# Optimization experiments

Hardware: AMD Instinct MI355X
Metric: run time of the kernel (lower is better)

## Reference

```python
import jax, jax.numpy as jnp
import numpy as np

N_AGENTS = 32
STATE_DIM = 512
EMBED = 64
BATCH = 32768


def setup_inputs() -> dict:
    key = jax.random.key(0)
    ks = jax.random.split(key, 16)
    g = lambda k, shape, fan_in: jax.random.normal(k, shape, jnp.float32) / np.sqrt(fan_in)
    return {
        "agent_qs": jax.random.normal(ks[0], (BATCH, N_AGENTS), jnp.float32),
        "states": jax.random.normal(ks[1], (BATCH, STATE_DIM), jnp.float32),
        # hyper_w1: Linear(state,E) -> ReLU -> Linear(E, n_agents*E)
        "w1_l1_w": g(ks[2], (EMBED, STATE_DIM), STATE_DIM),
        "w1_l1_b": jnp.zeros((EMBED,), jnp.float32),
        "w1_l2_w": g(ks[3], (N_AGENTS * EMBED, EMBED), EMBED),
        "w1_l2_b": jnp.zeros((N_AGENTS * EMBED,), jnp.float32),
        # hyper_w2: Linear(state,E) -> ReLU -> Linear(E, E)
        "w2_l1_w": g(ks[4], (EMBED, STATE_DIM), STATE_DIM),
        "w2_l1_b": jnp.zeros((EMBED,), jnp.float32),
        "w2_l2_w": g(ks[5], (EMBED, EMBED), EMBED),
        "w2_l2_b": jnp.zeros((EMBED,), jnp.float32),
        # hyper_b1: Linear(state, E)
        "b1_w": g(ks[6], (EMBED, STATE_DIM), STATE_DIM),
        "b1_b": jnp.zeros((EMBED,), jnp.float32),
        # hyper_b2: Linear(state,E) -> ReLU -> Linear(E, 1)
        "b2_l1_w": g(ks[7], (EMBED, STATE_DIM), STATE_DIM),
        "b2_l1_b": jnp.zeros((EMBED,), jnp.float32),
        "b2_l2_w": g(ks[8], (1, EMBED), EMBED),
        "b2_l2_b": jnp.zeros((1,), jnp.float32),
    }


def _linear(x, w, b):
    return x @ w.T + b


def reference(agent_qs, states,
              w1_l1_w, w1_l1_b, w1_l2_w, w1_l2_b,
              w2_l1_w, w2_l1_b, w2_l2_w, w2_l2_b,
              b1_w, b1_b, b2_l1_w, b2_l1_b, b2_l2_w, b2_l2_b):
    B = agent_qs.shape[0]
    # hypernetworks producing per-sample weights
    w1 = jnp.abs(_linear(jax.nn.relu(_linear(states, w1_l1_w, w1_l1_b)), w1_l2_w, w1_l2_b))
    w1 = w1.reshape(B, N_AGENTS, EMBED)                      # [B, A, E]
    b1 = _linear(states, b1_w, b1_b)                         # [B, E]
    hidden = jax.nn.elu(jnp.einsum('ba,bae->be', agent_qs, w1) + b1)  # [B, E]
    w2 = jnp.abs(_linear(jax.nn.relu(_linear(states, w2_l1_w, w2_l1_b)), w2_l2_w, w2_l2_b))  # [B, E]
    b2 = _linear(jax.nn.relu(_linear(states, b2_l1_w, b2_l1_b)), b2_l2_w, b2_l2_b)           # [B, 1]
    q_total = jnp.einsum('be,be->b', hidden, w2) + b2[:, 0]  # [B]
    return q_total
```

## Files before the change

kernel.cpp:

```cpp
#include <hip/hip_runtime.h>

typedef unsigned short u16;
typedef unsigned int u32;
typedef short bf16x8 __attribute__((ext_vector_type(8)));
typedef float f32x4 __attribute__((ext_vector_type(4)));
typedef u16 u16x4 __attribute__((ext_vector_type(4)));

#define NAG 32
#define STATE 512
#define EMBED 64
#define TB 64

#define OFF_W1L1 0
#define OFF_W2L1 32768
#define OFF_B1W  65536
#define OFF_B2L1 98304
#define OFF_W1L2 131072
#define OFF_W2L2 262144
#define WS_TOTAL 266240

#define WBUF_OFF 0
#define SB_OFF   16384
#define SB_STR   72
#define QST_OFF  20992
#define QST_STR  68
#define W1BS_OFF 23168
#define Y_OFF    25216
#define Y_STR    200
#define PBUF_OFF 0
#define PBUF_STR 72
#define PBUF_WV  (64 * 72)
#define QACC_OFF  38016
#define QACC2_OFF 38144
#define B2WV_OFF  38272
#define SMEM_U16  38400

__device__ __forceinline__ float bf2f(u16 u) {
    u32 i = ((u32)u) << 16; float f;
    __builtin_memcpy(&f, &i, 4); return f;
}
__device__ __forceinline__ u16 f2bf(float f) {
    u32 i; __builtin_memcpy(&i, &f, 4);
    return (u16)((i + 0x8000u) >> 16);
}
__device__ __forceinline__ bf16x8 ld8(const u16* p) {
    return *reinterpret_cast<const bf16x8*>(p);
}
__device__ __forceinline__ bf16x8 cvt8(f32x4 a, f32x4 b) {
    bf16x8 r;
#pragma unroll
    for (int i = 0; i < 4; ++i) r[i]     = (short)f2bf(a[i]);
#pragma unroll
    for (int i = 0; i < 4; ++i) r[i + 4] = (short)f2bf(b[i]);
    return r;
}
__device__ __forceinline__ void dma16(const void* g, void* l) {
    __builtin_amdgcn_global_load_lds(
        (const __attribute__((address_space(1))) u32*)g,
        (__attribute__((address_space(3))) u32*)l, 16, 0, 0);
}

__global__ __launch_bounds__(256) void cvt_weights(
    const float* __restrict__ w1l1w, const float* __restrict__ w2l1w,
    const float* __restrict__ b1w,   const float* __restrict__ b2l1w,
    const float* __restrict__ w1l2w, const float* __restrict__ w2l2w,
    u16* __restrict__ ws)
{
    int idx = blockIdx.x * 256 + threadIdx.x;
    const float* src; int off;
    if      (idx < OFF_W2L1)  { src = w1l1w; off = OFF_W1L1; }
    else if (idx < OFF_B1W)   { src = w2l1w; off = OFF_W2L1; }
    else if (idx < OFF_B2L1)  { src = b1w;   off = OFF_B1W;  }
    else if (idx < OFF_W1L2)  { src = b2l1w; off = OFF_B2L1; }
    else if (idx < OFF_W2L2)  { src = w1l2w; off = OFF_W1L2; }
    else if (idx < WS_TOTAL)  { src = w2l2w; off = OFF_W2L2; }
    else return;
    ws[idx] = f2bf(src[idx - off]);
}

__global__ __launch_bounds__(256, 2) void qmix_kernel(
    const float* __restrict__ qs,    const float* __restrict__ st,
    const u16*  __restrict__ wsb,
    const float* __restrict__ w1l1b, const float* __restrict__ w1l2b,
    const float* __restrict__ w2l1b, const float* __restrict__ w2l2b,
    const float* __restrict__ b1b,   const float* __restrict__ b2l1b,
    const float* __restrict__ b2l2w, const float* __restrict__ b2l2b,
    float* __restrict__ out)
{
    __shared__ u16 smem[SMEM_U16];
    float* qaccF  = (float*)(smem + QACC_OFF);
    float* qacc2F = (float*)(smem + QACC2_OFF);
    float* b2wvF  = (float*)(smem + B2WV_OFF);

    const int t    = threadIdx.x;
    const int wave = t >> 6, lane = t & 63;
    const int m = lane & 15, quad = lane >> 4;
    const int rsub = lane >> 3, cch = lane & 7;
    const int sc = cch ^ rsub;
    const int sbase = blockIdx.x * TB;

    if (t < 64) b2wvF[t] = b2l2w[t];
    {
        const float* qp = qs + (size_t)sbase * NAG + t * 8;
        f32x4 q0 = *reinterpret_cast<const f32x4*>(qp);
        f32x4 q1 = *reinterpret_cast<const f32x4*>(qp + 4);
        const int s = t >> 2, a0 = (t & 3) * 8;
#pragma unroll
        for (int j = 0; j < 4; ++j) smem[QST_OFF + (a0 + j) * QST_STR + s]     = f2bf(q0[j]);
#pragma unroll
        for (int j = 0; j < 4; ++j) smem[QST_OFF + (a0 + 4 + j) * QST_STR + s] = f2bf(q1[j]);
        f32x4 w0 = *reinterpret_cast<const f32x4*>(w1l2b + t * 8);
        f32x4 w1 = *reinterpret_cast<const f32x4*>(w1l2b + t * 8 + 4);
        *reinterpret_cast<bf16x8*>(&smem[W1BS_OFF + t * 8]) = cvt8(w0, w1);
    }

    const int ss1 = t >> 3, c8 = t & 7;
    const float* stb = st + (size_t)sbase * STATE;

    f32x4 acc[4][4] = {};
    for (int ks = 0; ks < 8; ++ks) {
        __syncthreads();
#pragma unroll
        for (int j = 0; j < 8; ++j)
            dma16(wsb + (size_t)(wave * 64 + j * 8 + rsub) * STATE + ks * 64 + sc * 8,
                  &smem[WBUF_OFF + (wave * 64 + j * 8) * 64]);
        {
            const float* g1 = stb + (size_t)ss1 * STATE + ks * 64 + c8 * 8;
            const float* g2 = g1 + (size_t)32 * STATE;
            f32x4 a0 = *reinterpret_cast<const f32x4*>(g1);
            f32x4 a1 = *reinterpret_cast<const f32x4*>(g1 + 4);
            f32x4 a2 = *reinterpret_cast<const f32x4*>(g2);
            f32x4 a3 = *reinterpret_cast<const f32x4*>(g2 + 4);
            *reinterpret_cast<bf16x8*>(&smem[SB_OFF + ss1 * SB_STR + c8 * 8])        = cvt8(a0, a1);
            *reinterpret_cast<bf16x8*>(&smem[SB_OFF + (ss1 + 32) * SB_STR + c8 * 8]) = cvt8(a2, a3);
        }
        __builtin_amdgcn_s_waitcnt(0);
        __syncthreads();
        bf16x8 wfr[4][2];
#pragma unroll
        for (int ot = 0; ot < 4; ++ot) {
            const int brow = wave * 64 + ot * 16 + m;
            wfr[ot][0] = ld8(&smem[WBUF_OFF + brow * 64 + ((quad ^ (brow & 7))) * 8]);
            wfr[ot][1] = ld8(&smem[WBUF_OFF + brow * 64 + (((quad + 4) ^ (brow & 7))) * 8]);
        }
#pragma unroll
        for (int st2 = 0; st2 < 4; ++st2) {
            const int row = st2 * 16 + m;
            bf16x8 af0 = ld8(&smem[SB_OFF + row * SB_STR + quad * 8]);
            bf16x8 af1 = ld8(&smem[SB_OFF + row * SB_STR + (quad + 4) * 8]);
#pragma unroll
            for (int ot = 0; ot < 4; ++ot)
                acc[st2][ot] = __builtin_amdgcn_mfma_f32_16x16x32_bf16(af0, wfr[ot][0], acc[st2][ot], 0, 0, 0);
#pragma unroll
            for (int ot = 0; ot < 4; ++ot)
                acc[st2][ot] = __builtin_amdgcn_mfma_f32_16x16x32_bf16(af1, wfr[ot][1], acc[st2][ot], 0, 0, 0);
        }
    }

    if (wave < 3) {
        const float* barr = (wave == 0) ? w1l1b : (wave == 1) ? w2l1b : b1b;
        const bool isrelu = (wave != 2);
        float wb[4];
#pragma unroll
        for (int ot = 0; ot < 4; ++ot) wb[ot] = barr[ot * 16 + m];
#pragma unroll
        for (int st2 = 0; st2 < 4; ++st2)
#pragma unroll
            for (int ot = 0; ot < 4; ++ot)
#pragma unroll
                for (int r = 0; r < 4; ++r) {
                    float v = acc[st2][ot][r] + wb[ot];
                    if (isrelu) v = fmaxf(v, 0.f);
                    smem[Y_OFF + (st2 * 16 + quad * 4 + r) * Y_STR + wave * 64 + ot * 16 + m] = f2bf(v);
                }
    } else {
        float wb[4], bw[4];
#pragma unroll
        for (int ot = 0; ot < 4; ++ot) wb[ot] = b2l1b[ot * 16 + m];
#pragma unroll
        for (int ot = 0; ot < 4; ++ot) bw[ot] = b2wvF[ot * 16 + m];
#pragma unroll
        for (int st2 = 0; st2 < 4; ++st2)
#pragma unroll
            for (int r = 0; r < 4; ++r) {
                float pd = 0.f;
#pragma unroll
                for (int ot = 0; ot < 4; ++ot)
                    pd += fmaxf(acc[st2][ot][r] + wb[ot], 0.f) * bw[ot];
#pragma unroll
                for (int off = 1; off < 16; off <<= 1) pd += __shfl_xor(pd, off, 64);
                if (m == 0) qacc2F[st2 * 16 + quad * 4 + r] = pd;
            }
    }
    __syncthreads();

    bf16x8 h1f[4][2];
#pragma unroll
    for (int st2 = 0; st2 < 4; ++st2) {
        h1f[st2][0] = ld8(&smem[Y_OFF + (st2 * 16 + m) * Y_STR + quad * 8]);
        h1f[st2][1] = ld8(&smem[Y_OFF + (st2 * 16 + m) * Y_STR + 32 + quad * 8]);
    }

    f32x4 hacc[4][4] = {};
    for (int j = 0; j < 8; ++j) {
        __syncthreads();
        const int a = wave * 8 + j;
#pragma unroll
        for (int jj = 0; jj < 8; ++jj)
            dma16(wsb + OFF_W1L2 + (size_t)(a * 64 + jj * 8 + rsub) * EMBED + sc * 8,
                  &smem[WBUF_OFF + (wave * 64 + jj * 8) * 64]);
        __builtin_amdgcn_s_waitcnt(0);
        __syncthreads();
        bf16x8 wf[4][2];
#pragma unroll
        for (int tp = 0; tp < 4; ++tp) {
            const int brow = wave * 64 + tp * 16 + m;
            wf[tp][0] = ld8(&smem[WBUF_OFF + brow * 64 + ((quad ^ (brow & 7))) * 8]);
            wf[tp][1] = ld8(&smem[WBUF_OFF + brow * 64 + (((quad + 4) ^ (brow & 7))) * 8]);
        }
        float bias[4];
#pragma unroll
        for (int tp = 0; tp < 4; ++tp) bias[tp] = bf2f(smem[W1BS_OFF + a * EMBED + tp * 16 + m]);
#pragma unroll
        for (int st2 = 0; st2 < 4; ++st2) {
            u16x4 qv = *reinterpret_cast<const u16x4*>(
                &smem[QST_OFF + a * QST_STR + st2 * 16 + quad * 4]);
#pragma unroll
            for (int tp = 0; tp < 4; ++tp) {
                f32x4 p = {};
                p = __builtin_amdgcn_mfma_f32_16x16x32_bf16(h1f[st2][0], wf[tp][0], p, 0, 0, 0);
                p = __builtin_amdgcn_mfma_f32_16x16x32_bf16(h1f[st2][1], wf[tp][1], p, 0, 0, 0);
#pragma unroll
                for (int r = 0; r < 4; ++r)
                    hacc[st2][tp][r] += bf2f((u16)qv[r]) * fabsf(p[r] + bias[tp]);
            }
        }
    }
    __syncthreads();

#pragma unroll
    for (int st2 = 0; st2 < 4; ++st2)
#pragma unroll
        for (int tp = 0; tp < 4; ++tp)
#pragma unroll
            for (int r = 0; r < 4; ++r)
                smem[PBUF_OFF + wave * PBUF_WV
                     + (st2 * 16 + quad * 4 + r) * PBUF_STR + tp * 16 + m]
                    = f2bf(hacc[st2][tp][r]);
    __syncthreads();

    {
        const int s  = wave * 16 + (lane & 15);
        const int eb = (lane >> 4) * 16;
        float v[16];
#pragma unroll
        for (int jj = 0; jj < 16; ++jj) v[jj] = 0.f;
#pragma unroll
        for (int pw = 0; pw < 4; ++pw) {
#pragma unroll
            for (int c = 0; c < 4; ++c) {
                u16x4 x = *reinterpret_cast<const u16x4*>(
                    &smem[PBUF_OFF + pw * PBUF_WV + s * PBUF_STR + eb + c * 4]);
#pragma unroll
                for (int jj = 0; jj < 4; ++jj) v[c * 4 + jj] += bf2f((u16)x[jj]);
            }
        }
        bf16x8 bv0 = ld8(&smem[Y_OFF + s * Y_STR + 128 + eb]);
        bf16x8 bv1 = ld8(&smem[Y_OFF + s * Y_STR + 128 + eb + 8]);
        bf16x8 o0, o1;
#pragma unroll
        for (int jj = 0; jj < 8; ++jj) {
            float h0 = v[jj] + bf2f((u16)bv0[jj]);
            h0 = (h0 > 0.f) ? h0 : (__expf(h0) - 1.f);
            o0[jj] = (short)f2bf(h0);
            float h1 = v[8 + jj] + bf2f((u16)bv1[jj]);
            h1 = (h1 > 0.f) ? h1 : (__expf(h1) - 1.f);
            o1[jj] = (short)f2bf(h1);
        }
        *reinterpret_cast<bf16x8*>(&smem[Y_OFF + s * Y_STR + 128 + eb])     = o0;
        *reinterpret_cast<bf16x8*>(&smem[Y_OFF + s * Y_STR + 128 + eb + 8]) = o1;
    }
    __syncthreads();

    {
        const int s0 = wave * 16;
        bf16x8 h2f0 = ld8(&smem[Y_OFF + (s0 + m) * Y_STR + 64 + quad * 8]);
        bf16x8 h2f1 = ld8(&smem[Y_OFF + (s0 + m) * Y_STR + 96 + quad * 8]);

        f32x4 qp = {};
#pragma unroll
        for (int tp = 0; tp < 4; ++tp) {
            const u16* wc = wsb + OFF_W2L2 + (size_t)(tp * 16 + m) * EMBED + quad * 8;
            bf16x8 c0 = ld8(wc);
            bf16x8 c1 = ld8(wc + 32);
            f32x4 p = {};
            p = __builtin_amdgcn_mfma_f32_16x16x32_bf16(h2f0, c0, p, 0, 0, 0);
            p = __builtin_amdgcn_mfma_f32_16x16x32_bf16(h2f1, c1, p, 0, 0, 0);
            const float bias = w2l2b[tp * 16 + m];
#pragma unroll
            for (int r = 0; r < 4; ++r)
                qp[r] += bf2f(smem[Y_OFF + (s0 + quad * 4 + r) * Y_STR + 128 + tp * 16 + m])
                         * fabsf(p[r] + bias);
        }
#pragma unroll
        for (int off = 1; off < 16; off <<= 1) {
#pragma unroll
            for (int r = 0; r < 4; ++r) qp[r] += __shfl_xor(qp[r], off, 64);
        }
        if (m == 0) {
#pragma unroll
            for (int r = 0; r < 4; ++r) qaccF[s0 + quad * 4 + r] = qp[r];
        }
    }
    __syncthreads();

    if (t < TB) out[sbase + t] = qaccF[t] + qacc2F[t] + b2l2b[0];
}

extern "C" void kernel_launch(void* const* d_in, const int* in_sizes, int n_in,
                              void* d_out, int out_size, void* d_ws, size_t ws_size,
                              hipStream_t stream)
{
    const float* qs    = (const float*)d_in[0];
    const float* st    = (const float*)d_in[1];
    const float* w1l1w = (const float*)d_in[2];
    const float* w1l1b = (const float*)d_in[3];
    const float* w1l2w = (const float*)d_in[4];
    const float* w1l2b = (const float*)d_in[5];
    const float* w2l1w = (const float*)d_in[6];
    const float* w2l1b = (const float*)d_in[7];
    const float* w2l2w = (const float*)d_in[8];
    const float* w2l2b = (const float*)d_in[9];
    const float* b1w   = (const float*)d_in[10];
    const float* b1b   = (const float*)d_in[11];
    const float* b2l1w = (const float*)d_in[12];
    const float* b2l1b = (const float*)d_in[13];
    const float* b2l2w = (const float*)d_in[14];
    const float* b2l2b = (const float*)d_in[15];

    u16* wsb = (u16*)d_ws;

    cvt_weights<<<(WS_TOTAL + 255) / 256, 256, 0, stream>>>(
        w1l1w, w2l1w, b1w, b2l1w, w1l2w, w2l2w, wsb);

    int B = in_sizes[0] / NAG;
    int grid = B / TB;
    qmix_kernel<<<grid, 256, 0, stream>>>(
        qs, st, wsb,
        w1l1b, w1l2b, w2l1b, w2l2b, b1b, b2l1b, b2l2w, b2l2b,
        (float*)d_out);
}
```

Before: 147.5 us.

## Double-buffer weight DMA and state staging across both GEMM loops

Splits each K-step into two half-tiles and double-buffers the weight tiles in LDS, issuing the async copy for the next half-tile before computing on the current one. State rows are prefetched into registers one step ahead and written into a second LDS buffer, and the first W1L2 tile is prefetched during the last state-GEMM step. This removes the wait-all-then-compute pattern per iteration, keeping one barrier per step. The b1 output moves to its own LDS region so the Y buffer shrinks. In exchange it uses more LDS and registers and fully unrolls 16-step loops, which may reduce occupancy or grow code size.

```diff
diff --git a/kernel.cpp b/kernel.cpp
--- a/kernel.cpp
+++ b/kernel.cpp
@@ -20,20 +20,23 @@
 #define WS_TOTAL 266240
 
 #define WBUF_OFF 0
+#define WBUF_SZ  8192
 #define SB_OFF   16384
 #define SB_STR   72
-#define QST_OFF  20992
+#define SB_BUF   4608
+#define B1V_OFF  20992
+#define QST_OFF  25600
 #define QST_STR  68
-#define W1BS_OFF 23168
-#define Y_OFF    25216
-#define Y_STR    200
+#define W1BS_OFF 27776
+#define Y_OFF    29824
+#define Y_STR    136
 #define PBUF_OFF 0
 #define PBUF_STR 72
-#define PBUF_WV  (64 * 72)
-#define QACC_OFF  38016
-#define QACC2_OFF 38144
-#define B2WV_OFF  38272
-#define SMEM_U16  38400
+#define PBUF_WV  4608
+#define QACC_OFF  38528
+#define QACC2_OFF 38656
+#define B2WV_OFF  38784
+#define SMEM_U16  38912
 
 __device__ __forceinline__ float bf2f(u16 u) {
     u32 i = ((u32)u) << 16; float f;
@@ -95,8 +98,8 @@
     const int t    = threadIdx.x;
     const int wave = t >> 6, lane = t & 63;
     const int m = lane & 15, quad = lane >> 4;
-    const int rsub = lane >> 3, cch = lane & 7;
-    const int sc = cch ^ rsub;
+    const int r8 = lane >> 3, c8l = lane & 7;
+    const int scx = c8l ^ r8;
     const int sbase = blockIdx.x * TB;
 
     if (t < 64) b2wvF[t] = b2l2w[t];
@@ -116,67 +119,105 @@
 
     const int ss1 = t >> 3, c8 = t & 7;
     const float* stb = st + (size_t)sbase * STATE;
+    {
+        const float* g1 = stb + (size_t)ss1 * STATE + c8 * 8;
+        const float* g2 = g1 + (size_t)32 * STATE;
+        f32x4 a0 = *reinterpret_cast<const f32x4*>(g1);
+        f32x4 a1 = *reinterpret_cast<const f32x4*>(g1 + 4);
+        f32x4 a2 = *reinterpret_cast<const f32x4*>(g2);
+        f32x4 a3 = *reinterpret_cast<const f32x4*>(g2 + 4);
+        *reinterpret_cast<bf16x8*>(&smem[SB_OFF + ss1 * SB_STR + c8 * 8])        = cvt8(a0, a1);
+        *reinterpret_cast<bf16x8*>(&smem[SB_OFF + (ss1 + 32) * SB_STR + c8 * 8]) = cvt8(a2, a3);
+    }
+#pragma unroll
+    for (int j = 0; j < 4; ++j)
+        dma16(wsb + (size_t)(wave * 64 + j * 8 + r8) * STATE + scx * 8,
+              &smem[WBUF_OFF + (wave * 32 + j * 8) * 64]);
+    __syncthreads();
 
     f32x4 acc[4][4] = {};
-    for (int ks = 0; ks < 8; ++ks) {
-        __syncthreads();
-#pragma unroll
-        for (int j = 0; j < 8; ++j)
-            dma16(wsb + (size_t)(wave * 64 + j * 8 + rsub) * STATE + ks * 64 + sc * 8,
-                  &smem[WBUF_OFF + (wave * 64 + j * 8) * 64]);
-        {
-            const float* g1 = stb + (size_t)ss1 * STATE + ks * 64 + c8 * 8;
+    f32x4 sa[4];
+#pragma unroll
+    for (int s = 0; s < 16; ++s) {
+        const int ks = s >> 1, h = s & 1, cur = s & 1, nxt = cur ^ 1;
+        if (s < 15) {
+            const int ks2 = (s + 1) >> 1, h2 = (s + 1) & 1;
+#pragma unroll
+            for (int j = 0; j < 4; ++j)
+                dma16(wsb + (size_t)(wave * 64 + h2 * 32 + j * 8 + r8) * STATE + ks2 * 64 + scx * 8,
+                      &smem[WBUF_OFF + nxt * WBUF_SZ + (wave * 32 + j * 8) * 64]);
+        } else {
+#pragma unroll
+            for (int j = 0; j < 4; ++j)
+                dma16(wsb + OFF_W1L2 + (size_t)(wave * 8 * 64 + j * 8 + r8) * EMBED + scx * 8,
+                      &smem[WBUF_OFF + nxt * WBUF_SZ + (wave * 32 + j * 8) * 64]);
+        }
+        if (h == 0 && ks < 7) {
+            const float* g1 = stb + (size_t)ss1 * STATE + (ks + 1) * 64 + c8 * 8;
             const float* g2 = g1 + (size_t)32 * STATE;
-            f32x4 a0 = *reinterpret_cast<const f32x4*>(g1);
-            f32x4 a1 = *reinterpret_cast<const f32x4*>(g1 + 4);
-            f32x4 a2 = *reinterpret_cast<const f32x4*>(g2);
-            f32x4 a3 = *reinterpret_cast<const f32x4*>(g2 + 4);
-            *reinterpret_cast<bf16x8*>(&smem[SB_OFF + ss1 * SB_STR + c8 * 8])        = cvt8(a0, a1);
-            *reinterpret_cast<bf16x8*>(&smem[SB_OFF + (ss1 + 32) * SB_STR + c8 * 8]) = cvt8(a2, a3);
-        }
-        __builtin_amdgcn_s_waitcnt(0);
-        __syncthreads();
-        bf16x8 wfr[4][2];
-#pragma unroll
-        for (int ot = 0; ot < 4; ++ot) {
-            const int brow = wave * 64 + ot * 16 + m;
-            wfr[ot][0] = ld8(&smem[WBUF_OFF + brow * 64 + ((quad ^ (brow & 7))) * 8]);
-            wfr[ot][1] = ld8(&smem[WBUF_OFF + brow * 64 + (((quad + 4) ^ (brow & 7))) * 8]);
+            sa[0] = *reinterpret_cast<const f32x4*>(g1);
+            sa[1] = *reinterpret_cast<const f32x4*>(g1 + 4);
+            sa[2] = *reinterpret_cast<const f32x4*>(g2);
+            sa[3] = *reinterpret_cast<const f32x4*>(g2 + 4);
+        }
+        const u16* wb  = &smem[WBUF_OFF + cur * WBUF_SZ];
+        const u16* sbc = &smem[SB_OFF + (ks & 1) * SB_BUF];
+        bf16x8 wf[2][2];
+#pragma unroll
+        for (int o = 0; o < 2; ++o) {
+            const int br = wave * 32 + o * 16 + m;
+            wf[o][0] = ld8(&wb[br * 64 + ((quad ^ (m & 7))) * 8]);
+            wf[o][1] = ld8(&wb[br * 64 + (((quad + 4) ^ (m & 7))) * 8]);
         }
 #pragma unroll
         for (int st2 = 0; st2 < 4; ++st2) {
             const int row = st2 * 16 + m;
-            bf16x8 af0 = ld8(&smem[SB_OFF + row * SB_STR + quad * 8]);
-            bf16x8 af1 = ld8(&smem[SB_OFF + row * SB_STR + (quad + 4) * 8]);
+            bf16x8 af0 = ld8(&sbc[row * SB_STR + quad * 8]);
+            bf16x8 af1 = ld8(&sbc[row * SB_STR + (quad + 4) * 8]);
+#pragma unroll
+            for (int o = 0; o < 2; ++o) {
+                acc[st2][h * 2 + o] = __builtin_amdgcn_mfma_f32_16x16x32_bf16(af0, wf[o][0], acc[st2][h * 2 + o], 0, 0, 0);
+                acc[st2][h * 2 + o] = __builtin_amdgcn_mfma_f32_16x16x32_bf16(af1, wf[o][1], acc[st2][h * 2 + o], 0, 0, 0);
+            }
+        }
+        if (h == 1 && ks < 7) {
+            u16* dst = &smem[SB_OFF + ((ks + 1) & 1) * SB_BUF];
+            *reinterpret_cast<bf16x8*>(&dst[ss1 * SB_STR + c8 * 8])        = cvt8(sa[0], sa[1]);
+            *reinterpret_cast<bf16x8*>(&dst[(ss1 + 32) * SB_STR + c8 * 8]) = cvt8(sa[2], sa[3]);
+        }
+        __syncthreads();
+    }
+
+    if (wave < 2) {
+        const float* barr = (wave == 0) ? w1l1b : w2l1b;
+        float wb4[4];
+#pragma unroll
+        for (int ot = 0; ot < 4; ++ot) wb4[ot] = barr[ot * 16 + m];
+#pragma unroll
+        for (int st2 = 0; st2 < 4; ++st2)
 #pragma unroll
             for (int ot = 0; ot < 4; ++ot)
-                acc[st2][ot] = __builtin_amdgcn_mfma_f32_16x16x32_bf16(af0, wfr[ot][0], acc[st2][ot], 0, 0, 0);
-#pragma unroll
-            for (int ot = 0; ot < 4; ++ot)
-                acc[st2][ot] = __builtin_amdgcn_mfma_f32_16x16x32_bf16(af1, wfr[ot][1], acc[st2][ot], 0, 0, 0);
-        }
-    }
-
-    if (wave < 3) {
-        const float* barr = (wave == 0) ? w1l1b : (wave == 1) ? w2l1b : b1b;
-        const bool isrelu = (wave != 2);
-        float wb[4];
-#pragma unroll
-        for (int ot = 0; ot < 4; ++ot) wb[ot] = barr[ot * 16 + m];
-#pragma unroll
-        for (int st2 = 0; st2 < 4; ++st2)
-#pragma unroll
-            for (int ot = 0; ot < 4; ++ot)
 #pragma unroll
                 for (int r = 0; r < 4; ++r) {
-                    float v = acc[st2][ot][r] + wb[ot];
-                    if (isrelu) v = fmaxf(v, 0.f);
+                    float v = fmaxf(acc[st2][ot][r] + wb4[ot], 0.f);
                     smem[Y_OFF + (st2 * 16 + quad * 4 + r) * Y_STR + wave * 64 + ot * 16 + m] = f2bf(v);
                 }
+    } else if (wave == 2) {
+        float wb4[4];
+#pragma unroll
+        for (int ot = 0; ot < 4; ++ot) wb4[ot] = b1b[ot * 16 + m];
+#pragma unroll
+        for (int st2 = 0; st2 < 4; ++st2)
+#pragma unroll
+            for (int ot = 0; ot < 4; ++ot)
+#pragma unroll
+                for (int r = 0; r < 4; ++r)
+                    smem[B1V_OFF + (st2 * 16 + quad * 4 + r) * SB_STR + ot * 16 + m]
+                        = f2bf(acc[st2][ot][r] + wb4[ot]);
     } else {
-        float wb[4], bw[4];
-#pragma unroll
-        for (int ot = 0; ot < 4; ++ot) wb[ot] = b2l1b[ot * 16 + m];
+        float wb4[4], bw[4];
+#pragma unroll
+        for (int ot = 0; ot < 4; ++ot) wb4[ot] = b2l1b[ot * 16 + m];
 #pragma unroll
         for (int ot = 0; ot < 4; ++ot) bw[ot] = b2wvF[ot * 16 + m];
 #pragma unroll
@@ -186,7 +227,7 @@
                 float pd = 0.f;
 #pragma unroll
                 for (int ot = 0; ot < 4; ++ot)
-                    pd += fmaxf(acc[st2][ot][r] + wb[ot], 0.f) * bw[ot];
+                    pd += fmaxf(acc[st2][ot][r] + wb4[ot], 0.f) * bw[ot];
 #pragma unroll
                 for (int off = 1; off < 16; off <<= 1) pd += __shfl_xor(pd, off, 64);
                 if (m == 0) qacc2F[st2 * 16 + quad * 4 + r] = pd;
@@ -202,41 +243,46 @@
     }
 
     f32x4 hacc[4][4] = {};
-    for (int j = 0; j < 8; ++j) {
-        __syncthreads();
-        const int a = wave * 8 + j;
-#pragma unroll
-        for (int jj = 0; jj < 8; ++jj)
-            dma16(wsb + OFF_W1L2 + (size_t)(a * 64 + jj * 8 + rsub) * EMBED + sc * 8,
-                  &smem[WBUF_OFF + (wave * 64 + jj * 8) * 64]);
-        __builtin_amdgcn_s_waitcnt(0);
-        __syncthreads();
-        bf16x8 wf[4][2];
-#pragma unroll
-        for (int tp = 0; tp < 4; ++tp) {
-            const int brow = wave * 64 + tp * 16 + m;
-            wf[tp][0] = ld8(&smem[WBUF_OFF + brow * 64 + ((quad ^ (brow & 7))) * 8]);
-            wf[tp][1] = ld8(&smem[WBUF_OFF + brow * 64 + (((quad + 4) ^ (brow & 7))) * 8]);
-        }
-        float bias[4];
-#pragma unroll
-        for (int tp = 0; tp < 4; ++tp) bias[tp] = bf2f(smem[W1BS_OFF + a * EMBED + tp * 16 + m]);
+#pragma unroll
+    for (int s = 0; s < 16; ++s) {
+        const int jb = s >> 1, hb = s & 1, cur = s & 1, nxt = cur ^ 1;
+        const int a = wave * 8 + jb;
+        if (s < 15) {
+            const int jb2 = (s + 1) >> 1, hb2 = (s + 1) & 1;
+            const int a2 = wave * 8 + jb2;
+#pragma unroll
+            for (int j = 0; j < 4; ++j)
+                dma16(wsb + OFF_W1L2 + (size_t)(a2 * 64 + hb2 * 32 + j * 8 + r8) * EMBED + scx * 8,
+                      &smem[WBUF_OFF + nxt * WBUF_SZ + (wave * 32 + j * 8) * 64]);
+        }
+        const u16* wb = &smem[WBUF_OFF + cur * WBUF_SZ];
+        bf16x8 wf[2][2];
+#pragma unroll
+        for (int o = 0; o < 2; ++o) {
+            const int br = wave * 32 + o * 16 + m;
+            wf[o][0] = ld8(&wb[br * 64 + ((quad ^ (m & 7))) * 8]);
+            wf[o][1] = ld8(&wb[br * 64 + (((quad + 4) ^ (m & 7))) * 8]);
+        }
+        float bias2[2];
+#pragma unroll
+        for (int o = 0; o < 2; ++o)
+            bias2[o] = bf2f(smem[W1BS_OFF + a * EMBED + (hb * 2 + o) * 16 + m]);
 #pragma unroll
         for (int st2 = 0; st2 < 4; ++st2) {
             u16x4 qv = *reinterpret_cast<const u16x4*>(
                 &smem[QST_OFF + a * QST_STR + st2 * 16 + quad * 4]);
 #pragma unroll
-            for (int tp = 0; tp < 4; ++tp) {
+            for (int o = 0; o < 2; ++o) {
                 f32x4 p = {};
-                p = __builtin_amdgcn_mfma_f32_16x16x32_bf16(h1f[st2][0], wf[tp][0], p, 0, 0, 0);
-                p = __builtin_amdgcn_mfma_f32_16x16x32_bf16(h1f[st2][1], wf[tp][1], p, 0, 0, 0);
+                p = __builtin_amdgcn_mfma_f32_16x16x32_bf16(h1f[st2][0], wf[o][0], p, 0, 0, 0);
+                p = __builtin_amdgcn_mfma_f32_16x16x32_bf16(h1f[st2][1], wf[o][1], p, 0, 0, 0);
 #pragma unroll
                 for (int r = 0; r < 4; ++r)
-                    hacc[st2][tp][r] += bf2f((u16)qv[r]) * fabsf(p[r] + bias[tp]);
+                    hacc[st2][hb * 2 + o][r] += bf2f((u16)qv[r]) * fabsf(p[r] + bias2[o]);
             }
         }
-    }
-    __syncthreads();
+        __syncthreads();
+    }
 
 #pragma unroll
     for (int st2 = 0; st2 < 4; ++st2)
@@ -265,8 +311,8 @@
                 for (int jj = 0; jj < 4; ++jj) v[c * 4 + jj] += bf2f((u16)x[jj]);
             }
         }
-        bf16x8 bv0 = ld8(&smem[Y_OFF + s * Y_STR + 128 + eb]);
-        bf16x8 bv1 = ld8(&smem[Y_OFF + s * Y_STR + 128 + eb + 8]);
+        bf16x8 bv0 = ld8(&smem[B1V_OFF + s * SB_STR + eb]);
+        bf16x8 bv1 = ld8(&smem[B1V_OFF + s * SB_STR + eb + 8]);
         bf16x8 o0, o1;
 #pragma unroll
         for (int jj = 0; jj < 8; ++jj) {
@@ -277,8 +323,8 @@
             h1 = (h1 > 0.f) ? h1 : (__expf(h1) - 1.f);
             o1[jj] = (short)f2bf(h1);
         }
-        *reinterpret_cast<bf16x8*>(&smem[Y_OFF + s * Y_STR + 128 + eb])     = o0;
-        *reinterpret_cast<bf16x8*>(&smem[Y_OFF + s * Y_STR + 128 + eb + 8]) = o1;
+        *reinterpret_cast<bf16x8*>(&smem[B1V_OFF + s * SB_STR + eb])     = o0;
+        *reinterpret_cast<bf16x8*>(&smem[B1V_OFF + s * SB_STR + eb + 8]) = o1;
     }
     __syncthreads();
 
@@ -299,7 +345,7 @@
             const float bias = w2l2b[tp * 16 + m];
 #pragma unroll
             for (int r = 0; r < 4; ++r)
-                qp[r] += bf2f(smem[Y_OFF + (s0 + quad * 4 + r) * Y_STR + 128 + tp * 16 + m])
+                qp[r] += bf2f(smem[B1V_OFF + (s0 + quad * 4 + r) * SB_STR + tp * 16 + m])
                          * fabsf(p[r] + bias);
         }
 #pragma unroll
```

Result: no change. 145.3 us (-1.5%).
